# Kernel optimization log

Hardware: AMD Instinct MI355X
Metric: run time of the kernel (lower is better)

Reference implementation:

```python
import jax, jax.numpy as jnp
import numpy as np
import math

DEPTH = 4
IN_FEATURES = 1024
LEAF_WIDTH = 256
OUT_FEATURES = 1024
BATCH = 8192
N_LEAVES = 2 ** DEPTH      # 16
N_NODES = 2 ** DEPTH - 1   # 15


def setup_inputs() -> dict:
    key = jax.random.key(0)
    ks = jax.random.split(key, 8)
    l1 = 1.0 / math.sqrt(IN_FEATURES)
    l2 = 1.0 / math.sqrt(LEAF_WIDTH)
    u = lambda k, shape, f: jax.random.uniform(k, shape, jnp.float32, -f, f)
    return {
        "x": jax.random.normal(ks[0], (BATCH, IN_FEATURES), jnp.float32),
        "node_weights": u(ks[1], (N_NODES, IN_FEATURES), l1),
        "node_biases": u(ks[2], (N_NODES, 1), l1),
        "w1s": u(ks[3], (N_LEAVES, IN_FEATURES, LEAF_WIDTH), l1),
        "b1s": u(ks[4], (N_LEAVES, LEAF_WIDTH), l1),
        "w2s": u(ks[5], (N_LEAVES, LEAF_WIDTH, OUT_FEATURES), l2),
        "b2s": u(ks[6], (N_LEAVES, OUT_FEATURES), l2),
    }


def reference(x, node_weights, node_biases, w1s, b1s, w2s, b2s):
    # Soft tree-gated routing (training_forward, soft decisions, no leak).
    B = x.shape[0]
    mixture = jnp.ones((B, N_LEAVES), dtype=x.dtype)
    for d in range(DEPTH):  # static small loop over tree depth
        plat, nxt = 2 ** d - 1, 2 ** (d + 1) - 1
        n = 2 ** d
        w = node_weights[plat:nxt]          # (n, F)
        b = node_biases[plat:nxt]           # (n, 1)
        logits = x @ w.T + b.T              # (B, n)
        be = jax.nn.sigmoid(logits)
        # interleave (1-be, be) along node axis -> (B, 2n, 1)
        mod = jnp.stack([1.0 - be, be], axis=-1).reshape(B, 2 * n, 1)
        mixture = (mixture.reshape(B, 2 * n, N_LEAVES // (2 * n)) * mod).reshape(B, N_LEAVES)
    # Per-leaf two-layer MLP, then mixture-weighted sum over leaves.
    h = jnp.einsum("bf,lfh->blh", x, w1s) + b1s[None]          # (B, L, H)
    a = jax.nn.relu(h)
    y = jnp.einsum("blh,lho->blo", a, w2s) + b2s[None]          # (B, L, O)
    return jnp.sum(y * mixture[:, :, None], axis=1)             # (B, O)
```

## Files before the change

kernel.cpp:

```cpp
#include <hip/hip_runtime.h>
#include <hip/hip_bf16.h>
#include <math.h>

#define BATCH 8192
#define INF   1024
#define LEAFW 256
#define OUTF  1024
#define NLEAF 16
#define NNODE 15
#define NTOT  4096
#define KEXT  4160

typedef __bf16 bf16;
typedef __bf16 bf16x4 __attribute__((ext_vector_type(4)));
typedef __bf16 bf16x8 __attribute__((ext_vector_type(8)));
typedef float  f32x4  __attribute__((ext_vector_type(4)));

__global__ __launch_bounds__(256) void prep_gk(
    const float* __restrict__ w1, const float* __restrict__ w2,
    const float* __restrict__ b2s, const float4* __restrict__ x4,
    const float4* __restrict__ nw4, const float* __restrict__ nb,
    bf16* __restrict__ W1T, bf16* __restrict__ W2T, float* __restrict__ mg,
    bf16* __restrict__ Aact, bf16x4* __restrict__ Xbf4) {
  __shared__ float tile[64][65];
  int b = blockIdx.x;
  int t = threadIdx.x;

  if (b < 2048) {
    const float* src;
    bf16* dst;
    int srcld, dstld, r0, c0;
    if (b < 1024) {
      int l = b >> 6, rem = b & 63;
      r0 = (rem >> 2) * 64;
      c0 = (rem & 3) * 64;
      src = w1 + (size_t)l * INF * LEAFW;
      srcld = LEAFW;
      dst = W1T + (size_t)l * LEAFW * INF;
      dstld = INF;
    } else {
      int bb = b - 1024;
      int l = bb >> 6, rem = bb & 63;
      r0 = (rem >> 4) * 64;
      c0 = (rem & 15) * 64;
      src = w2 + (size_t)l * LEAFW * OUTF;
      srcld = OUTF;
      dst = W2T + l * LEAFW;
      dstld = KEXT;
    }
    int fr = t >> 4, hc4 = (t & 15) * 4;
#pragma unroll
    for (int p = 0; p < 4; ++p) {
      float4 v = *reinterpret_cast<const float4*>(
          &src[(size_t)(r0 + fr + p * 16) * srcld + c0 + hc4]);
      tile[fr + p * 16][hc4 + 0] = v.x;
      tile[fr + p * 16][hc4 + 1] = v.y;
      tile[fr + p * 16][hc4 + 2] = v.z;
      tile[fr + p * 16][hc4 + 3] = v.w;
    }
    __syncthreads();
#pragma unroll
    for (int p = 0; p < 2; ++p) {
      int s = t + p * 256;
      int h = s >> 3, fc = (s & 7) * 8;
      bf16x8 o;
#pragma unroll
      for (int e = 0; e < 8; ++e) o[e] = (bf16)tile[fc + e][h];
      *reinterpret_cast<bf16x8*>(&dst[(size_t)(c0 + h) * dstld + r0 + fc]) = o;
    }
    return;
  }

  if (b < 2304) {
    int i = (b - 2048) * 256 + t;
    int o = i >> 6, j = i & 63;
    W2T[(size_t)o * KEXT + NTOT + j] =
        (j < NLEAF) ? (bf16)b2s[(size_t)j * OUTF + o] : (bf16)0.f;
    return;
  }

  int row  = (b - 2304) * 4 + (t >> 6);
  int lane = t & 63;
  const float4* xr4 = x4 + (size_t)row * (INF / 4);

  float p[NNODE];
#pragma unroll
  for (int j = 0; j < NNODE; ++j) p[j] = 0.f;
#pragma unroll
  for (int c = 0; c < INF / 256; ++c) {
    int idx = c * 64 + lane;
    float4 xv = xr4[idx];
#pragma unroll
    for (int j = 0; j < NNODE; ++j) {
      float4 wv = nw4[j * (INF / 4) + idx];
      p[j] += xv.x * wv.x + xv.y * wv.y + xv.z * wv.z + xv.w * wv.w;
    }
    bf16x4 o = {(bf16)xv.x, (bf16)xv.y, (bf16)xv.z, (bf16)xv.w};
    Xbf4[(size_t)row * (INF / 4) + idx] = o;
  }
#pragma unroll
  for (int j = 0; j < NNODE; ++j) {
    float v = p[j];
#pragma unroll
    for (int off = 32; off > 0; off >>= 1) v += __shfl_xor(v, off);
    p[j] = 1.f / (1.f + expf(-(v + nb[j])));
  }
  float mixv[NLEAF];
#pragma unroll
  for (int L = 0; L < NLEAF; ++L) {
    int n1 = 1 + (L >> 3), n2 = 3 + (L >> 2), n3 = 7 + (L >> 1);
    float m = ((L >> 3) & 1) ? p[0] : (1.f - p[0]);
    m *= ((L >> 2) & 1) ? p[n1] : (1.f - p[n1]);
    m *= ((L >> 1) & 1) ? p[n2] : (1.f - p[n2]);
    m *= (L & 1) ? p[n3] : (1.f - p[n3]);
    mixv[L] = m;
  }
  bf16* arow = Aact + (size_t)row * KEXT + NTOT;
  if (lane == 0) {
#pragma unroll
    for (int L = 0; L < NLEAF; ++L) {
      mg[row * NLEAF + L] = mixv[L];
      arow[L] = (bf16)mixv[L];
    }
  }
  if (lane >= 16) arow[lane] = (bf16)0.f;
}

template <int N>
__device__ __forceinline__ void wait_vmcnt() {
  asm volatile("s_waitcnt vmcnt(%0)" ::"n"(N) : "memory");
}
__device__ __forceinline__ void barrier_fence() {
  asm volatile("" ::: "memory");
  __builtin_amdgcn_s_barrier();
  asm volatile("" ::: "memory");
}

__global__ __launch_bounds__(512, 2) void gemm1_kernel(
    const bf16* __restrict__ A, const bf16* __restrict__ BT,
    const float* __restrict__ bias, const float* __restrict__ mg,
    bf16* __restrict__ outB) {
  constexpr int NT  = INF / 64;
  constexpr int ASZ = 256 * 64;
  constexpr int BSZ = 256 * 64;
  __shared__ __align__(16) bf16 As[2 * ASZ];
  __shared__ __align__(16) bf16 Bs[2 * BSZ];

  const int t = threadIdx.x, lane = t & 63, w = t >> 6;
  const int wm = w >> 2, wn = w & 3;
  const int orig = blockIdx.x;
  const int xcd  = orig & 7, idx = orig >> 3;
  const int bm = ((xcd << 2) + (idx & 3)) * 256;
  const int bn = (idx >> 2) * 256;
  const int lr = t >> 3, cs = t & 7;
  const int scol = ((cs ^ (lr & 7)) << 3);

  auto stageA = [&](int kt, int h, int buf) {
#pragma unroll
    for (int q = 0; q < 2; ++q) {
      const bf16* src =
          A + (size_t)(bm + h * 128 + q * 64 + lr) * INF + kt * 64 + scol;
      __builtin_amdgcn_global_load_lds(
          (const __attribute__((address_space(1))) void*)src,
          (__attribute__((address_space(3))) void*)((char*)As +
                                                    buf * (ASZ * 2) +
                                                    h * 16384 + q * 8192 +
                                                    t * 16),
          16, 0, 0);
    }
  };
  auto stageB = [&](int kt, int h, int buf) {
#pragma unroll
    for (int q = 0; q < 2; ++q) {
      const bf16* src =
          BT + (size_t)(bn + h * 128 + q * 64 + lr) * INF + kt * 64 + scol;
      __builtin_amdgcn_global_load_lds(
          (const __attribute__((address_space(1))) void*)src,
          (__attribute__((address_space(3))) void*)((char*)Bs +
                                                    buf * (BSZ * 2) +
                                                    h * 16384 + q * 8192 +
                                                    t * 16),
          16, 0, 0);
    }
  };
  auto rdA = [&](int buf, int i, int kk) -> bf16x8 {
    int r  = wm * 64 + (i & 3) * 16 + (lane & 15);
    int ch = ((kk << 2) + (lane >> 4)) ^ (lane & 7);
    return *reinterpret_cast<const bf16x8*>(
        &As[buf * ASZ + (i >> 2) * 8192 + r * 64 + ch * 8]);
  };
  auto rdB = [&](int buf, int j, int kk) -> bf16x8 {
    int r  = wn * 32 + (j & 1) * 16 + (lane & 15);
    int ch = ((kk << 2) + (lane >> 4)) ^ (lane & 7);
    return *reinterpret_cast<const bf16x8*>(
        &Bs[buf * BSZ + (j >> 1) * 8192 + r * 64 + ch * 8]);
  };

  f32x4 acc[8][4];
#pragma unroll
  for (int i = 0; i < 8; ++i)
#pragma unroll
    for (int j = 0; j < 4; ++j) acc[i][j] = (f32x4){0.f, 0.f, 0.f, 0.f};

  stageA(0, 0, 0);
  stageB(0, 0, 0);
  stageB(0, 1, 0);
  stageA(0, 1, 0);
  wait_vmcnt<4>();
  barrier_fence();

  for (int kt = 0; kt < NT; ++kt) {
    const int cur = kt & 1, nxt = cur ^ 1;
    const int k1 = kt + 1 < NT ? kt + 1 : NT - 1;
    bf16x8 af0[4][2], af1[4][2], bq0[2][2], bq1[2][2];

#pragma unroll
    for (int i = 0; i < 4; ++i)
#pragma unroll
      for (int kk = 0; kk < 2; ++kk) af0[i][kk] = rdA(cur, i, kk);
#pragma unroll
    for (int j = 0; j < 2; ++j)
#pragma unroll
      for (int kk = 0; kk < 2; ++kk) bq0[j][kk] = rdB(cur, j, kk);
    stageA(k1, 0, nxt);
    __builtin_amdgcn_s_setprio(1);
#pragma unroll
    for (int kk = 0; kk < 2; ++kk)
#pragma unroll
      for (int i = 0; i < 4; ++i)
#pragma unroll
        for (int j = 0; j < 2; ++j)
          acc[i][j] = __builtin_amdgcn_mfma_f32_16x16x32_bf16(
              af0[i][kk], bq0[j][kk], acc[i][j], 0, 0, 0);
    __builtin_amdgcn_s_setprio(0);
    wait_vmcnt<4>();
    barrier_fence();

#pragma unroll
    for (int j = 0; j < 2; ++j)
#pragma unroll
      for (int kk = 0; kk < 2; ++kk) bq1[j][kk] = rdB(cur, 2 + j, kk);
    stageB(k1, 0, nxt);
    __builtin_amdgcn_s_setprio(1);
#pragma unroll
    for (int kk = 0; kk < 2; ++kk)
#pragma unroll
      for (int i = 0; i < 4; ++i)
#pragma unroll
        for (int j = 0; j < 2; ++j)
          acc[i][2 + j] = __builtin_amdgcn_mfma_f32_16x16x32_bf16(
              af0[i][kk], bq1[j][kk], acc[i][2 + j], 0, 0, 0);
    __builtin_amdgcn_s_setprio(0);
    wait_vmcnt<4>();
    barrier_fence();

#pragma unroll
    for (int i = 0; i < 4; ++i)
#pragma unroll
      for (int kk = 0; kk < 2; ++kk) af1[i][kk] = rdA(cur, 4 + i, kk);
    stageB(k1, 1, nxt);
    __builtin_amdgcn_s_setprio(1);
#pragma unroll
    for (int kk = 0; kk < 2; ++kk)
#pragma unroll
      for (int i = 0; i < 4; ++i)
#pragma unroll
        for (int j = 0; j < 2; ++j)
          acc[4 + i][2 + j] = __builtin_amdgcn_mfma_f32_16x16x32_bf16(
              af1[i][kk], bq1[j][kk], acc[4 + i][2 + j], 0, 0, 0);
    __builtin_amdgcn_s_setprio(0);
    wait_vmcnt<6>();
    barrier_fence();

    stageA(k1, 1, nxt);
    __builtin_amdgcn_s_setprio(1);
#pragma unroll
    for (int kk = 0; kk < 2; ++kk)
#pragma unroll
      for (int i = 0; i < 4; ++i)
#pragma unroll
        for (int j = 0; j < 2; ++j)
          acc[4 + i][j] = __builtin_amdgcn_mfma_f32_16x16x32_bf16(
              af1[i][kk], bq0[j][kk], acc[4 + i][j], 0, 0, 0);
    __builtin_amdgcn_s_setprio(0);
    wait_vmcnt<4>();
    barrier_fence();
  }

  const int leaf = bn >> 8;
#pragma unroll
  for (int i = 0; i < 8; ++i) {
    int rb = bm + (i >> 2) * 128 + wm * 64 + (i & 3) * 16 + ((lane >> 4) << 2);
#pragma unroll
    for (int rr = 0; rr < 4; ++rr) {
      const int grow = rb + rr;
      const float g  = mg[grow * NLEAF + leaf];
#pragma unroll
      for (int j = 0; j < 4; ++j) {
        const int gcol =
            bn + (j >> 1) * 128 + wn * 32 + (j & 1) * 16 + (lane & 15);
        float v = acc[i][j][rr] + bias[gcol];
        v = v > 0.f ? v : 0.f;
        outB[(size_t)grow * KEXT + gcol] = (bf16)(v * g);
      }
    }
  }
}

__global__ __launch_bounds__(512, 2) void gemm2_kernel(
    const bf16* __restrict__ A, const bf16* __restrict__ BT,
    float* __restrict__ outF) {
  constexpr int NT  = KEXT / 64;
  constexpr int ASZ = 128 * 64;
  constexpr int BSZ = 256 * 64;
  __shared__ __align__(16) bf16 As[2 * ASZ];
  __shared__ __align__(16) bf16 Bs[2 * BSZ];

  const int t = threadIdx.x, lane = t & 63, w = t >> 6;
  const int wm = w >> 2, wn = w & 3;
  const int orig = blockIdx.x;
  const int swz  = (orig & 7) * 32 + (orig >> 3);
  const int bm = (swz >> 2) * 128, bn = (swz & 3) * 256;
  const int lr = t >> 3, cs = t & 7;
  const int scol = ((cs ^ (lr & 7)) << 3);

  auto stageA = [&](int kt, int buf) {
#pragma unroll
    for (int q = 0; q < 2; ++q) {
      const bf16* src = A + (size_t)(bm + q * 64 + lr) * KEXT + kt * 64 + scol;
      __builtin_amdgcn_global_load_lds(
          (const __attribute__((address_space(1))) void*)src,
          (__attribute__((address_space(3))) void*)((char*)As +
                                                    buf * (ASZ * 2) +
                                                    q * 8192 + t * 16),
          16, 0, 0);
    }
  };
  auto stageB = [&](int kt, int h, int buf) {
#pragma unroll
    for (int q = 0; q < 2; ++q) {
      const bf16* src =
          BT + (size_t)(bn + h * 128 + q * 64 + lr) * KEXT + kt * 64 + scol;
      __builtin_amdgcn_global_load_lds(
          (const __attribute__((address_space(1))) void*)src,
          (__attribute__((address_space(3))) void*)((char*)Bs +
                                                    buf * (BSZ * 2) +
                                                    h * 16384 + q * 8192 +
                                                    t * 16),
          16, 0, 0);
    }
  };
  auto rdA = [&](int buf, int i, int kk) -> bf16x8 {
    int r  = (i >> 1) * 64 + wm * 32 + (i & 1) * 16 + (lane & 15);
    int ch = ((kk << 2) + (lane >> 4)) ^ (lane & 7);
    return *reinterpret_cast<const bf16x8*>(&As[buf * ASZ + r * 64 + ch * 8]);
  };
  auto rdB = [&](int buf, int j, int kk) -> bf16x8 {
    int r  = wn * 32 + (j & 1) * 16 + (lane & 15);
    int ch = ((kk << 2) + (lane >> 4)) ^ (lane & 7);
    return *reinterpret_cast<const bf16x8*>(
        &Bs[buf * BSZ + (j >> 1) * 8192 + r * 64 + ch * 8]);
  };

  f32x4 acc[4][4];
#pragma unroll
  for (int i = 0; i < 4; ++i)
#pragma unroll
    for (int j = 0; j < 4; ++j) acc[i][j] = (f32x4){0.f, 0.f, 0.f, 0.f};

  stageA(0, 0);
  stageB(0, 0, 0);
  stageB(0, 1, 0);
  wait_vmcnt<2>();
  barrier_fence();

  for (int kt = 0; kt < NT; ++kt) {
    const int cur = kt & 1, nxt = cur ^ 1;
    const int k1 = kt + 1 < NT ? kt + 1 : NT - 1;
    bf16x8 af[4][2], bq0[2][2], bq1[2][2];

#pragma unroll
    for (int i = 0; i < 4; ++i)
#pragma unroll
      for (int kk = 0; kk < 2; ++kk) af[i][kk] = rdA(cur, i, kk);
#pragma unroll
    for (int j = 0; j < 2; ++j)
#pragma unroll
      for (int kk = 0; kk < 2; ++kk) bq0[j][kk] = rdB(cur, j, kk);
    stageA(k1, nxt);
    stageB(k1, 0, nxt);
    __builtin_amdgcn_s_setprio(1);
#pragma unroll
    for (int kk = 0; kk < 2; ++kk)
#pragma unroll
      for (int i = 0; i < 4; ++i)
#pragma unroll
        for (int j = 0; j < 2; ++j)
          acc[i][j] = __builtin_amdgcn_mfma_f32_16x16x32_bf16(
              af[i][kk], bq0[j][kk], acc[i][j], 0, 0, 0);
    __builtin_amdgcn_s_setprio(0);
    wait_vmcnt<4>();
    barrier_fence();

#pragma unroll
    for (int j = 0; j < 2; ++j)
#pragma unroll
      for (int kk = 0; kk < 2; ++kk) bq1[j][kk] = rdB(cur, 2 + j, kk);
    stageB(k1, 1, nxt);
    __builtin_amdgcn_s_setprio(1);
#pragma unroll
    for (int kk = 0; kk < 2; ++kk)
#pragma unroll
      for (int i = 0; i < 4; ++i)
#pragma unroll
        for (int j = 0; j < 2; ++j)
          acc[i][2 + j] = __builtin_amdgcn_mfma_f32_16x16x32_bf16(
              af[i][kk], bq1[j][kk], acc[i][2 + j], 0, 0, 0);
    __builtin_amdgcn_s_setprio(0);
    wait_vmcnt<2>();
    barrier_fence();
  }

#pragma unroll
  for (int i = 0; i < 4; ++i) {
    int rb = bm + (i >> 1) * 64 + wm * 32 + (i & 1) * 16 + ((lane >> 4) << 2);
#pragma unroll
    for (int rr = 0; rr < 4; ++rr) {
      const int grow = rb + rr;
#pragma unroll
      for (int j = 0; j < 4; ++j) {
        const int gcol =
            bn + (j >> 1) * 128 + wn * 32 + (j & 1) * 16 + (lane & 15);
        outF[(size_t)grow * OUTF + gcol] = acc[i][j][rr];
      }
    }
  }
}

extern "C" void kernel_launch(void* const* d_in, const int* in_sizes, int n_in,
                              void* d_out, int out_size, void* d_ws,
                              size_t ws_size, hipStream_t stream) {
  const float* x   = (const float*)d_in[0];
  const float* nw  = (const float*)d_in[1];
  const float* nb  = (const float*)d_in[2];
  const float* w1s = (const float*)d_in[3];
  const float* b1s = (const float*)d_in[4];
  const float* w2s = (const float*)d_in[5];
  const float* b2s = (const float*)d_in[6];
  float* out = (float*)d_out;

  char* ws = (char*)d_ws;
  bf16*  Xbf  = (bf16*)(ws);
  bf16*  W1T  = (bf16*)(ws + 16777216);
  bf16*  W2T  = (bf16*)(ws + 25165824);
  float* mg   = (float*)(ws + 33685504);
  bf16*  Aact = (bf16*)(ws + 34209792);

  prep_gk<<<dim3(4352), 256, 0, stream>>>(
      w1s, w2s, b2s, (const float4*)x, (const float4*)nw, nb, W1T, W2T, mg,
      Aact, (bf16x4*)Xbf);

  gemm1_kernel<<<dim3(512), 512, 0, stream>>>(Xbf, W1T, b1s, mg, Aact);
  gemm2_kernel<<<dim3(256), 512, 0, stream>>>(Aact, W2T, out);
}
```

Baseline: 264.0 us.

## Make gemm1 persistent over four 128-row M tiles with streamed K

Gemm1 moves from 512 blocks, each computing a 256x256 tile, to 256 persistent blocks. Each block walks four consecutive 128x256 tiles in one flat 64-step K pipeline and writes its epilogue after every 16 steps. This halves the accumulator registers, removes the wave-tail with one block per CU slot, and keeps the loader running across tiles. The cost is reloading the B tile for each M tile (less reuse per block) and a full vmcnt drain plus barrier at each tile boundary.

```diff
diff --git a/kernel.cpp b/kernel.cpp
--- a/kernel.cpp
+++ b/kernel.cpp
@@ -136,12 +136,12 @@
   asm volatile("" ::: "memory");
 }
 
-__global__ __launch_bounds__(512, 2) void gemm1_kernel(
+__global__ __launch_bounds__(512, 2) void g1_pers(
     const bf16* __restrict__ A, const bf16* __restrict__ BT,
     const float* __restrict__ bias, const float* __restrict__ mg,
     bf16* __restrict__ outB) {
-  constexpr int NT  = INF / 64;
-  constexpr int ASZ = 256 * 64;
+  constexpr int NS  = 64;
+  constexpr int ASZ = 128 * 64;
   constexpr int BSZ = 256 * 64;
   __shared__ __align__(16) bf16 As[2 * ASZ];
   __shared__ __align__(16) bf16 Bs[2 * BSZ];
@@ -150,22 +150,20 @@
   const int wm = w >> 2, wn = w & 3;
   const int orig = blockIdx.x;
   const int xcd  = orig & 7, idx = orig >> 3;
-  const int bm = ((xcd << 2) + (idx & 3)) * 256;
-  const int bn = (idx >> 2) * 256;
+  const int bn   = (idx & 15) * 256;
+  const int bm0  = (xcd * 2 + (idx >> 4)) * 512;
   const int lr = t >> 3, cs = t & 7;
   const int scol = ((cs ^ (lr & 7)) << 3);
 
-  auto stageA = [&](int kt, int h, int buf) {
+  auto stageA = [&](int vbm, int kt, int buf) {
 #pragma unroll
     for (int q = 0; q < 2; ++q) {
-      const bf16* src =
-          A + (size_t)(bm + h * 128 + q * 64 + lr) * INF + kt * 64 + scol;
+      const bf16* src = A + (size_t)(vbm + q * 64 + lr) * INF + kt * 64 + scol;
       __builtin_amdgcn_global_load_lds(
           (const __attribute__((address_space(1))) void*)src,
           (__attribute__((address_space(3))) void*)((char*)As +
                                                     buf * (ASZ * 2) +
-                                                    h * 16384 + q * 8192 +
-                                                    t * 16),
+                                                    q * 8192 + t * 16),
           16, 0, 0);
     }
   };
@@ -184,10 +182,9 @@
     }
   };
   auto rdA = [&](int buf, int i, int kk) -> bf16x8 {
-    int r  = wm * 64 + (i & 3) * 16 + (lane & 15);
+    int r  = (i >> 1) * 64 + wm * 32 + (i & 1) * 16 + (lane & 15);
     int ch = ((kk << 2) + (lane >> 4)) ^ (lane & 7);
-    return *reinterpret_cast<const bf16x8*>(
-        &As[buf * ASZ + (i >> 2) * 8192 + r * 64 + ch * 8]);
+    return *reinterpret_cast<const bf16x8*>(&As[buf * ASZ + r * 64 + ch * 8]);
   };
   auto rdB = [&](int buf, int j, int kk) -> bf16x8 {
     int r  = wn * 32 + (j & 1) * 16 + (lane & 15);
@@ -196,33 +193,37 @@
         &Bs[buf * BSZ + (j >> 1) * 8192 + r * 64 + ch * 8]);
   };
 
-  f32x4 acc[8][4];
-#pragma unroll
-  for (int i = 0; i < 8; ++i)
+  f32x4 acc[4][4];
+#pragma unroll
+  for (int i = 0; i < 4; ++i)
 #pragma unroll
     for (int j = 0; j < 4; ++j) acc[i][j] = (f32x4){0.f, 0.f, 0.f, 0.f};
 
-  stageA(0, 0, 0);
+  const int leaf = bn >> 8;
+
+  stageA(bm0, 0, 0);
   stageB(0, 0, 0);
   stageB(0, 1, 0);
-  stageA(0, 1, 0);
-  wait_vmcnt<4>();
+  wait_vmcnt<2>();
   barrier_fence();
 
-  for (int kt = 0; kt < NT; ++kt) {
-    const int cur = kt & 1, nxt = cur ^ 1;
-    const int k1 = kt + 1 < NT ? kt + 1 : NT - 1;
-    bf16x8 af0[4][2], af1[4][2], bq0[2][2], bq1[2][2];
+  for (int s = 0; s < NS; ++s) {
+    const int cur = s & 1, nxt = cur ^ 1;
+    const int u   = (s + 1 < NS) ? s + 1 : NS - 1;
+    const int ukt = u & 15;
+    const int ubm = bm0 + (u >> 4) * 128;
+    bf16x8 af[4][2], bq0[2][2], bq1[2][2];
 
 #pragma unroll
     for (int i = 0; i < 4; ++i)
 #pragma unroll
-      for (int kk = 0; kk < 2; ++kk) af0[i][kk] = rdA(cur, i, kk);
+      for (int kk = 0; kk < 2; ++kk) af[i][kk] = rdA(cur, i, kk);
 #pragma unroll
     for (int j = 0; j < 2; ++j)
 #pragma unroll
       for (int kk = 0; kk < 2; ++kk) bq0[j][kk] = rdB(cur, j, kk);
-    stageA(k1, 0, nxt);
+    stageA(ubm, ukt, nxt);
+    stageB(ukt, 0, nxt);
     __builtin_amdgcn_s_setprio(1);
 #pragma unroll
     for (int kk = 0; kk < 2; ++kk)
@@ -231,7 +232,7 @@
 #pragma unroll
         for (int j = 0; j < 2; ++j)
           acc[i][j] = __builtin_amdgcn_mfma_f32_16x16x32_bf16(
-              af0[i][kk], bq0[j][kk], acc[i][j], 0, 0, 0);
+              af[i][kk], bq0[j][kk], acc[i][j], 0, 0, 0);
     __builtin_amdgcn_s_setprio(0);
     wait_vmcnt<4>();
     barrier_fence();
@@ -240,7 +241,7 @@
     for (int j = 0; j < 2; ++j)
 #pragma unroll
       for (int kk = 0; kk < 2; ++kk) bq1[j][kk] = rdB(cur, 2 + j, kk);
-    stageB(k1, 0, nxt);
+    stageB(ukt, 1, nxt);
     __builtin_amdgcn_s_setprio(1);
 #pragma unroll
     for (int kk = 0; kk < 2; ++kk)
@@ -249,60 +250,37 @@
 #pragma unroll
         for (int j = 0; j < 2; ++j)
           acc[i][2 + j] = __builtin_amdgcn_mfma_f32_16x16x32_bf16(
-              af0[i][kk], bq1[j][kk], acc[i][2 + j], 0, 0, 0);
+              af[i][kk], bq1[j][kk], acc[i][2 + j], 0, 0, 0);
     __builtin_amdgcn_s_setprio(0);
-    wait_vmcnt<4>();
+    wait_vmcnt<2>();
     barrier_fence();
 
-#pragma unroll
-    for (int i = 0; i < 4; ++i)
-#pragma unroll
-      for (int kk = 0; kk < 2; ++kk) af1[i][kk] = rdA(cur, 4 + i, kk);
-    stageB(k1, 1, nxt);
-    __builtin_amdgcn_s_setprio(1);
-#pragma unroll
-    for (int kk = 0; kk < 2; ++kk)
+    if ((s & 15) == 15) {
+      const int tbm = bm0 + (s >> 4) * 128;
+#pragma unroll
+      for (int i = 0; i < 4; ++i) {
+        int rb =
+            tbm + (i >> 1) * 64 + wm * 32 + (i & 1) * 16 + ((lane >> 4) << 2);
+#pragma unroll
+        for (int rr = 0; rr < 4; ++rr) {
+          const int grow = rb + rr;
+          const float g  = mg[grow * NLEAF + leaf];
+#pragma unroll
+          for (int j = 0; j < 4; ++j) {
+            const int gcol =
+                bn + (j >> 1) * 128 + wn * 32 + (j & 1) * 16 + (lane & 15);
+            float v = acc[i][j][rr] + bias[gcol];
+            v = v > 0.f ? v : 0.f;
+            outB[(size_t)grow * KEXT + gcol] = (bf16)(v * g);
+          }
+        }
+      }
 #pragma unroll
       for (int i = 0; i < 4; ++i)
 #pragma unroll
-        for (int j = 0; j < 2; ++j)
-          acc[4 + i][2 + j] = __builtin_amdgcn_mfma_f32_16x16x32_bf16(
-              af1[i][kk], bq1[j][kk], acc[4 + i][2 + j], 0, 0, 0);
-    __builtin_amdgcn_s_setprio(0);
-    wait_vmcnt<6>();
-    barrier_fence();
-
-    stageA(k1, 1, nxt);
-    __builtin_amdgcn_s_setprio(1);
-#pragma unroll
-    for (int kk = 0; kk < 2; ++kk)
-#pragma unroll
-      for (int i = 0; i < 4; ++i)
-#pragma unroll
-        for (int j = 0; j < 2; ++j)
-          acc[4 + i][j] = __builtin_amdgcn_mfma_f32_16x16x32_bf16(
-              af1[i][kk], bq0[j][kk], acc[4 + i][j], 0, 0, 0);
-    __builtin_amdgcn_s_setprio(0);
-    wait_vmcnt<4>();
-    barrier_fence();
-  }
-
-  const int leaf = bn >> 8;
-#pragma unroll
-  for (int i = 0; i < 8; ++i) {
-    int rb = bm + (i >> 2) * 128 + wm * 64 + (i & 3) * 16 + ((lane >> 4) << 2);
-#pragma unroll
-    for (int rr = 0; rr < 4; ++rr) {
-      const int grow = rb + rr;
-      const float g  = mg[grow * NLEAF + leaf];
-#pragma unroll
-      for (int j = 0; j < 4; ++j) {
-        const int gcol =
-            bn + (j >> 1) * 128 + wn * 32 + (j & 1) * 16 + (lane & 15);
-        float v = acc[i][j][rr] + bias[gcol];
-        v = v > 0.f ? v : 0.f;
-        outB[(size_t)grow * KEXT + gcol] = (bf16)(v * g);
-      }
+        for (int j = 0; j < 4; ++j) acc[i][j] = (f32x4){0.f, 0.f, 0.f, 0.f};
+      wait_vmcnt<0>();
+      barrier_fence();
     }
   }
 }
@@ -460,6 +438,6 @@
       w1s, w2s, b2s, (const float4*)x, (const float4*)nw, nb, W1T, W2T, mg,
       Aact, (bf16x4*)Xbf);
 
-  gemm1_kernel<<<dim3(512), 512, 0, stream>>>(Xbf, W1T, b1s, mg, Aact);
+  g1_pers<<<dim3(256), 512, 0, stream>>>(Xbf, W1T, b1s, mg, Aact);
   gemm2_kernel<<<dim3(256), 512, 0, stream>>>(Aact, W2T, out);
 }
```

New measurement: 265.9 us. No clear change (+0.7%).
